# Kernel optimization log

Hardware: AMD Instinct MI355X
Metric: run time of the kernel (lower is better)

## Reference

```python
import jax, jax.numpy as jnp
import numpy as np

N_NODES = 100000
N_EDGES = 1200000
IN_DIM, HID_DIM, LAT_DIM = 128, 64, 32


def gcn_conv(x, W, b, src, dst, n_nodes):
    # PyG GCNConv with add_self_loops=True, symmetric normalization.
    # src/dst already include self loops.
    h = x @ W  # [N, out]
    deg = jax.ops.segment_sum(jnp.ones_like(dst, dtype=h.dtype), dst,
                              num_segments=n_nodes)  # includes self loop -> >=1
    dinv = jax.lax.rsqrt(deg)
    norm = dinv[src] * dinv[dst]  # [E]
    msg = h[src] * norm[:, None]  # gather + scale, [E, out]
    out = jax.ops.segment_sum(msg, dst, num_segments=n_nodes)  # scatter-add
    return out + b


def setup_inputs() -> dict:
    key = jax.random.key(0)
    ks = jax.random.split(key, 9)
    x = jax.random.normal(ks[0], (N_NODES, IN_DIM), dtype=jnp.float32)
    edge_index = jax.random.randint(ks[1], (2, N_EDGES), 0, N_NODES, dtype=jnp.int32)
    s1 = 1.0 / np.sqrt(IN_DIM)
    s2 = 1.0 / np.sqrt(HID_DIM)
    W1 = jax.random.uniform(ks[2], (IN_DIM, HID_DIM), jnp.float32, -s1, s1)
    b1 = jnp.zeros((HID_DIM,), jnp.float32)
    Wm = jax.random.uniform(ks[3], (HID_DIM, LAT_DIM), jnp.float32, -s2, s2)
    bm = jnp.zeros((LAT_DIM,), jnp.float32)
    Wv = jax.random.uniform(ks[4], (HID_DIM, LAT_DIM), jnp.float32, -s2, s2)
    bv = jnp.zeros((LAT_DIM,), jnp.float32)
    noise = jax.random.normal(ks[5], (N_NODES, LAT_DIM), dtype=jnp.float32)
    return {"x": x, "edge_index": edge_index, "W1": W1, "b1": b1,
            "Wm": Wm, "bm": bm, "Wv": Wv, "bv": bv, "noise": noise}


def reference(x, edge_index, W1, b1, Wm, bm, Wv, bv, noise):
    n = x.shape[0]
    loops = jnp.arange(n, dtype=edge_index.dtype)
    src = jnp.concatenate([edge_index[0], loops])
    dst = jnp.concatenate([edge_index[1], loops])
    h = jnp.tanh(gcn_conv(x, W1, b1, src, dst, n))
    mean = gcn_conv(h, Wm, bm, src, dst, n)
    logvar = gcn_conv(h, Wv, bv, src, dst, n)
    z = noise * jnp.exp(0.5 * logvar) + mean
    return (z, mean, logvar)
```

## Files before the change

kernel.cpp:

```cpp
#include <hip/hip_runtime.h>
#include <math.h>

#define TILE 4096
#define CSHIFT 11
#define CMASK 2047
#define NCMAX 64

typedef __attribute__((ext_vector_type(8))) short bf16x8;
typedef __attribute__((ext_vector_type(4))) float f32x4;


__device__ __forceinline__ unsigned int pack_bf16(float a, float b) {
  unsigned int ua = __float_as_uint(a);
  ua += 0x7FFFu + ((ua >> 16) & 1u);
  unsigned int ub = __float_as_uint(b);
  ub += 0x7FFFu + ((ub >> 16) & 1u);
  return (ua >> 16) | (ub & 0xFFFF0000u);
}

__device__ __forceinline__ void add8(float* acc, uint4 hv) {
  unsigned int u[4] = {hv.x, hv.y, hv.z, hv.w};
#pragma unroll
  for (int i = 0; i < 4; ++i) {
    acc[2 * i]     += __uint_as_float(u[i] << 16);
    acc[2 * i + 1] += __uint_as_float(u[i] & 0xFFFF0000u);
  }
}

__device__ __forceinline__ void fma4(float4& acc, float s, const float4& w) {
  acc.x = fmaf(s, w.x, acc.x);
  acc.y = fmaf(s, w.y, acc.y);
  acc.z = fmaf(s, w.z, acc.z);
  acc.w = fmaf(s, w.w, acc.w);
}


__global__ void zero_kernel(int* __restrict__ p, int n) {
  int i = blockIdx.x * blockDim.x + threadIdx.x;
  if (i < n) p[i] = 0;
}

__global__ __launch_bounds__(256) void coarse_hist_kernel(const int* __restrict__ dst,
    int* __restrict__ ccnt, int e) {
  __shared__ int h[NCMAX];
  if (threadIdx.x < NCMAX) h[threadIdx.x] = 0;
  __syncthreads();
  for (int i = blockIdx.x * 256 + threadIdx.x; i < e; i += gridDim.x * 256)
    atomicAdd(&h[dst[i] >> CSHIFT], 1);
  __syncthreads();
  if (threadIdx.x < NCMAX && h[threadIdx.x])
    atomicAdd(&ccnt[threadIdx.x * 16], h[threadIdx.x]);
}

__global__ __launch_bounds__(64) void coarse_scan_kernel(const int* __restrict__ ccnt,
    int* __restrict__ coff, int* __restrict__ ccur, int* __restrict__ off,
    int nc, int n, int e) {
  int t = threadIdx.x;
  int v = (t < nc) ? ccnt[t * 16] : 0;
  int incl = v;
#pragma unroll
  for (int ofs = 1; ofs < 64; ofs <<= 1) {
    int w = __shfl_up(incl, ofs);
    if (t >= ofs) incl += w;
  }
  int excl = incl - v;
  if (t < nc) { coff[t] = excl; ccur[t * 16] = excl; }
  if (t == nc - 1) coff[nc] = incl;
  if (t == 0) off[n] = e;
}

__global__ __launch_bounds__(256) void coarse_partition_kernel(const int* __restrict__ src,
    const int* __restrict__ dst, int* __restrict__ ccur,
    unsigned int* __restrict__ packed, int e) {
  __shared__ unsigned int stage[TILE];
  __shared__ unsigned char bid[TILE];
  __shared__ int hist[NCMAX], excl[NCMAX], gbase[NCMAX], lcur[NCMAX];
  int ntiles = (e + TILE - 1) / TILE;
  for (int tile = blockIdx.x; tile < ntiles; tile += gridDim.x) {
    int i0 = tile * TILE;
    int cnt = e - i0; if (cnt > TILE) cnt = TILE;
    if (threadIdx.x < NCMAX) hist[threadIdx.x] = 0;
    __syncthreads();
    int myS[16], myD[16];
#pragma unroll
    for (int k = 0; k < 16; ++k) {
      int li = threadIdx.x + k * 256;
      if (li < cnt) {
        myS[k] = src[i0 + li];
        myD[k] = dst[i0 + li];
        atomicAdd(&hist[myD[k] >> CSHIFT], 1);
      }
    }
    __syncthreads();
    if (threadIdx.x < NCMAX) {
      int t = threadIdx.x;
      int v = hist[t];
      int incl = v;
#pragma unroll
      for (int ofs = 1; ofs < 64; ofs <<= 1) {
        int w = __shfl_up(incl, ofs);
        if (t >= ofs) incl += w;
      }
      excl[t] = incl - v;
      lcur[t] = incl - v;
    }
    __syncthreads();
#pragma unroll
    for (int k = 0; k < 16; ++k) {
      int li = threadIdx.x + k * 256;
      if (li < cnt) {
        int c = myD[k] >> CSHIFT;
        int p = atomicAdd(&lcur[c], 1);
        stage[p] = (unsigned int)myS[k] | ((unsigned int)(myD[k] & CMASK) << 17);
        bid[p] = (unsigned char)c;
      }
    }
    __syncthreads();
    if (threadIdx.x < NCMAX) {
      int t = threadIdx.x;
      int cc = lcur[t] - excl[t];
      gbase[t] = cc ? atomicAdd(&ccur[t * 16], cc) : 0;
    }
    __syncthreads();
    for (int i = threadIdx.x; i < cnt; i += 256) {
      int c = bid[i];
      packed[gbase[c] + (i - excl[c])] = stage[i];
    }
    __syncthreads();
  }
}

__global__ __launch_bounds__(512) void csr_fine_kernel(const unsigned int* __restrict__ packed,
    const int* __restrict__ coff, int* __restrict__ off, float* __restrict__ dinv,
    int* __restrict__ csr, int n) {
  __shared__ int lh[2048];
  __shared__ int lsum[512];
  int b = blockIdx.x;
  int t = threadIdx.x;
  int e0 = coff[b], e1 = coff[b + 1];
  int node0 = b << CSHIFT;
  for (int i = t; i < 2048; i += 512) lh[i] = 0;
  __syncthreads();
  for (int i = e0 + t; i < e1; i += 512) atomicAdd(&lh[packed[i] >> 17], 1);
  __syncthreads();
  int base = t * 4;
  int v0 = lh[base], v1 = lh[base + 1], v2 = lh[base + 2], v3 = lh[base + 3];
  int tsum = v0 + v1 + v2 + v3;
  lsum[t] = tsum;
  __syncthreads();
  for (int ofs = 1; ofs < 512; ofs <<= 1) {
    int add = (t >= ofs) ? lsum[t - ofs] : 0;
    __syncthreads();
    lsum[t] += add;
    __syncthreads();
  }
  int ex = lsum[t] - tsum;
  int exc0 = ex, exc1 = ex + v0, exc2 = ex + v0 + v1, exc3 = ex + v0 + v1 + v2;
  lh[base] = exc0; lh[base + 1] = exc1; lh[base + 2] = exc2; lh[base + 3] = exc3;
  int node = node0 + base;
  if (node < n)     { off[node]     = e0 + exc0; dinv[node]     = rsqrtf((float)(v0 + 1)); }
  if (node + 1 < n) { off[node + 1] = e0 + exc1; dinv[node + 1] = rsqrtf((float)(v1 + 1)); }
  if (node + 2 < n) { off[node + 2] = e0 + exc2; dinv[node + 2] = rsqrtf((float)(v2 + 1)); }
  if (node + 3 < n) { off[node + 3] = e0 + exc3; dinv[node + 3] = rsqrtf((float)(v3 + 1)); }
  __syncthreads();
  for (int i = e0 + t; i < e1; i += 512) {
    unsigned int p = packed[i];
    int nl = p >> 17;
    int pos = atomicAdd(&lh[nl], 1);
    csr[e0 + pos] = (int)(p & 0x1FFFFu);
  }
}

__global__ __launch_bounds__(256) void gemm1_kernel(const float* __restrict__ x,
    const float* __restrict__ W1, const float* __restrict__ dinv,
    unsigned int* __restrict__ h1, int n) {
  __shared__ unsigned int xs[64 * 64];
  __shared__ unsigned int wt[64 * 64];
  for (int i = threadIdx.x; i < 4096; i += 256) {
    int c = i & 63, kp = i >> 6;
    float a = W1[(2 * kp) * 64 + c];
    float b = W1[(2 * kp + 1) * 64 + c];
    int slot = kp >> 2;
    int slotS = slot ^ (c & 7);
    wt[c * 64 + slotS * 4 + (kp & 3)] = pack_bf16(a, b);
  }
  int row0 = blockIdx.x * 64;
  int nrow = n - row0; if (nrow > 64) nrow = 64;
  for (int i = threadIdx.x; i < 64 * 32; i += 256) {
    int r = i >> 5, q = i & 31;
    float4 v = make_float4(0.f, 0.f, 0.f, 0.f);
    if (r < nrow) v = ((const float4*)(x + (size_t)(row0 + r) * 128))[q];
    int slot = q >> 1;
    int slotS = slot ^ (r & 7);
    int bi = r * 64 + slotS * 4 + (q & 1) * 2;
    xs[bi]     = pack_bf16(v.x, v.y);
    xs[bi + 1] = pack_bf16(v.z, v.w);
  }
  __syncthreads();
  int lane = threadIdx.x & 63;
  int w = threadIdx.x >> 6;
  int rl = lane & 15;
  int g = lane >> 4;
  f32x4 acc[4];
#pragma unroll
  for (int i = 0; i < 4; ++i) acc[i] = (f32x4){0.f, 0.f, 0.f, 0.f};
#pragma unroll
  for (int ks = 0; ks < 4; ++ks) {
    int as = ((ks * 4 + g) ^ (rl & 7)) * 4;
    bf16x8 af = *reinterpret_cast<const bf16x8*>(&xs[(w * 16 + rl) * 64 + as]);
#pragma unroll
    for (int nt = 0; nt < 4; ++nt) {
      int col = nt * 16 + rl;
      int bs = ((ks * 4 + g) ^ (col & 7)) * 4;
      bf16x8 bfr = *reinterpret_cast<const bf16x8*>(&wt[col * 64 + bs]);
      acc[nt] = __builtin_amdgcn_mfma_f32_16x16x32_bf16(af, bfr, acc[nt], 0, 0, 0);
    }
  }
#pragma unroll
  for (int i = 0; i < 4; ++i) {
    int row = row0 + w * 16 + g * 4 + i;
    float dv = (row < n) ? dinv[row] : 0.f;
#pragma unroll
    for (int nt = 0; nt < 4; ++nt) {
      float val = dv * acc[nt][i];
      float pv = __shfl_xor(val, 1);
      if (!(lane & 1) && row < n) {
        h1[(size_t)row * 32 + nt * 8 + (rl >> 1)] = pack_bf16(val, pv);
      }
    }
  }
}

template <int EPI>
__global__ __launch_bounds__(256) void agg_kernel(const uint4* __restrict__ h4,
    const int* __restrict__ off, const int* __restrict__ csr,
    const float* __restrict__ dinv, const float* __restrict__ bias,
    unsigned int* __restrict__ out, int n) {
  int lane = threadIdx.x & 63;
  int nd = lane >> 5;
  int j  = (lane >> 1) & 15;
  int fl = lane & 1;
  int node = blockIdx.x * 8 + (threadIdx.x >> 6) * 2 + nd;
  bool valid = node < n;
  float acc[32];
#pragma unroll
  for (int i = 0; i < 32; ++i) acc[i] = 0.f;
  if (valid) {
    if (j == 0) {
      const uint4* hp = &h4[(size_t)node * 8 + fl * 4];
      uint4 a = hp[0], b = hp[1], c = hp[2], d = hp[3];
      add8(acc, a); add8(acc + 8, b); add8(acc + 16, c); add8(acc + 24, d);
    }
    int e1 = off[node + 1];
    for (int ee = off[node] + j; ee < e1; ee += 16) {
      int s = __builtin_nontemporal_load(&csr[ee]);
      const uint4* hp = &h4[(size_t)s * 8 + fl * 4];
      uint4 a = hp[0], b = hp[1], c = hp[2], d = hp[3];
      add8(acc, a); add8(acc + 8, b); add8(acc + 16, c); add8(acc + 24, d);
    }
  }
#pragma unroll
  for (int i = 0; i < 16; ++i) {
    float tlo = acc[i]      + __shfl_xor(acc[i], 2);
    float thi = acc[i + 16] + __shfl_xor(acc[i + 16], 2);
    acc[i] = (j & 1) ? thi : tlo;
  }
#pragma unroll
  for (int i = 0; i < 8; ++i) {
    float tlo = acc[i]     + __shfl_xor(acc[i], 4);
    float thi = acc[i + 8] + __shfl_xor(acc[i + 8], 4);
    acc[i] = (j & 2) ? thi : tlo;
  }
#pragma unroll
  for (int i = 0; i < 4; ++i) {
    float tlo = acc[i]     + __shfl_xor(acc[i], 8);
    float thi = acc[i + 4] + __shfl_xor(acc[i + 4], 8);
    acc[i] = (j & 4) ? thi : tlo;
  }
#pragma unroll
  for (int i = 0; i < 2; ++i) {
    float tlo = acc[i]     + __shfl_xor(acc[i], 16);
    float thi = acc[i + 2] + __shfl_xor(acc[i + 2], 16);
    acc[i] = (j & 8) ? thi : tlo;
  }
  int b0 = j & 1, b1 = (j >> 1) & 1, b2 = (j >> 2) & 1, b3 = (j >> 3) & 1;
  int f0 = fl * 32 + 16 * b0 + 8 * b1 + 4 * b2 + 2 * b3;
  if (valid) {
    float di = dinv[node];
    float v0, v1;
    if (EPI) {
      v0 = di * tanhf(fmaf(di, acc[0], bias[f0]));
      v1 = di * tanhf(fmaf(di, acc[1], bias[f0 + 1]));
    } else {
      v0 = di * acc[0];
      v1 = di * acc[1];
    }
    out[(size_t)node * 32 + (f0 >> 1)] = pack_bf16(v0, v1);
  }
}

__global__ __launch_bounds__(256) void final_kernel(const unsigned int* __restrict__ aggb,
    const float* __restrict__ Wm, const float* __restrict__ bm,
    const float* __restrict__ Wv, const float* __restrict__ bv,
    const float* __restrict__ noise, float* __restrict__ outZ,
    float* __restrict__ outM, float* __restrict__ outLv, int n) {
  __shared__ float WmS[64 * 32];
  __shared__ float WvS[64 * 32];
  __shared__ float aggS[64 * 68];
  for (int i = threadIdx.x; i < 64 * 8; i += 256) {
    ((float4*)WmS)[i] = ((const float4*)Wm)[i];
    ((float4*)WvS)[i] = ((const float4*)Wv)[i];
  }
  int row0 = blockIdx.x * 64;
  int nrow = n - row0; if (nrow > 64) nrow = 64;
  for (int i = threadIdx.x; i < 64 * 16; i += 256) {
    int r = i >> 4, g = i & 15;
    uint2 u = make_uint2(0u, 0u);
    if (r < nrow) u = ((const uint2*)aggb)[(size_t)(row0 + r) * 16 + g];
    float* d = &aggS[r * 68 + g * 4];
    d[0] = __uint_as_float(u.x << 16);
    d[1] = __uint_as_float(u.x & 0xFFFF0000u);
    d[2] = __uint_as_float(u.y << 16);
    d[3] = __uint_as_float(u.y & 0xFFFF0000u);
  }
  __syncthreads();
  int c4 = (threadIdx.x & 7) * 4;
  int r2 = (threadIdx.x >> 3) * 2;
  float4 am[2], av[2];
#pragma unroll
  for (int i = 0; i < 2; ++i) {
    am[i] = make_float4(0.f, 0.f, 0.f, 0.f);
    av[i] = make_float4(0.f, 0.f, 0.f, 0.f);
  }
#pragma unroll 4
  for (int kq = 0; kq < 16; ++kq) {
    float4 xa[2], wm[4], wv[4];
#pragma unroll
    for (int i = 0; i < 2; ++i) xa[i] = *(const float4*)&aggS[(r2 + i) * 68 + kq * 4];
#pragma unroll
    for (int q = 0; q < 4; ++q) {
      wm[q] = *(const float4*)&WmS[(kq * 4 + q) * 32 + c4];
      wv[q] = *(const float4*)&WvS[(kq * 4 + q) * 32 + c4];
    }
#pragma unroll
    for (int i = 0; i < 2; ++i) {
      fma4(am[i], xa[i].x, wm[0]); fma4(am[i], xa[i].y, wm[1]);
      fma4(am[i], xa[i].z, wm[2]); fma4(am[i], xa[i].w, wm[3]);
      fma4(av[i], xa[i].x, wv[0]); fma4(av[i], xa[i].y, wv[1]);
      fma4(av[i], xa[i].z, wv[2]); fma4(av[i], xa[i].w, wv[3]);
    }
  }
  float4 bmv = *(const float4*)&bm[c4];
  float4 bvv = *(const float4*)&bv[c4];
#pragma unroll
  for (int i = 0; i < 2; ++i) {
    int row = row0 + r2 + i;
    if (row < n) {
      float4 m = am[i]; m.x += bmv.x; m.y += bmv.y; m.z += bmv.z; m.w += bmv.w;
      float4 v = av[i]; v.x += bvv.x; v.y += bvv.y; v.z += bvv.z; v.w += bvv.w;
      size_t oi = (size_t)row * 8 + (threadIdx.x & 7);
      float4 nz = ((const float4*)noise)[oi];
      float4 z;
      z.x = fmaf(nz.x, expf(0.5f * v.x), m.x);
      z.y = fmaf(nz.y, expf(0.5f * v.y), m.y);
      z.z = fmaf(nz.z, expf(0.5f * v.z), m.z);
      z.w = fmaf(nz.w, expf(0.5f * v.w), m.w);
      ((float4*)outZ)[oi] = z;
      ((float4*)outM)[oi] = m;
      ((float4*)outLv)[oi] = v;
    }
  }
}


extern "C" void kernel_launch(void* const* d_in, const int* in_sizes, int n_in,
                              void* d_out, int out_size, void* d_ws, size_t ws_size,
                              hipStream_t stream) {
  const float* x     = (const float*)d_in[0];
  const int*   edge  = (const int*)d_in[1];
  const float* W1    = (const float*)d_in[2];
  const float* b1    = (const float*)d_in[3];
  const float* Wm    = (const float*)d_in[4];
  const float* bm    = (const float*)d_in[5];
  const float* Wv    = (const float*)d_in[6];
  const float* bv    = (const float*)d_in[7];
  const float* noise = (const float*)d_in[8];
  int n = in_sizes[0] / 128;
  int e = in_sizes[1] / 2;
  const int* src = edge;
  const int* dst = edge + e;
  int nc = (n + CMASK) >> CSHIFT;

  int* ccnt = (int*)d_ws;
  int* ccur = ccnt + NCMAX * 16;
  int* coff = ccur + NCMAX * 16;
  int* off  = coff + (NCMAX + 4);
  float* dinv = (float*)(off + ((n + 4) & ~3));
  unsigned int* packed = (unsigned int*)(dinv + ((n + 3) & ~3));
  int* csr  = (int*)(packed + ((e + 3) & ~3));
  unsigned int* h1b = (unsigned int*)(csr + ((e + 3) & ~3));
  unsigned int* hb  = h1b + (size_t)n * 32;
  unsigned int* aggb = hb + (size_t)n * 32;

  float* outZ  = (float*)d_out;
  float* outM  = outZ + (size_t)n * 32;
  float* outLv = outM + (size_t)n * 32;

  int ntiles = (e + TILE - 1) / TILE;

  zero_kernel<<<(NCMAX * 16 + 255) / 256, 256, 0, stream>>>(ccnt, NCMAX * 16);
  coarse_hist_kernel<<<256, 256, 0, stream>>>(dst, ccnt, e);
  coarse_scan_kernel<<<1, 64, 0, stream>>>(ccnt, coff, ccur, off, nc, n, e);
  coarse_partition_kernel<<<ntiles, 256, 0, stream>>>(src, dst, ccur, packed, e);
  csr_fine_kernel<<<nc, 512, 0, stream>>>(packed, coff, off, dinv, csr, n);
  gemm1_kernel<<<(n + 63) / 64, 256, 0, stream>>>(x, W1, dinv, h1b, n);
  agg_kernel<1><<<(n + 7) / 8, 256, 0, stream>>>((const uint4*)h1b, off, csr, dinv, b1, hb, n);
  agg_kernel<0><<<(n + 7) / 8, 256, 0, stream>>>((const uint4*)hb, off, csr, dinv, b1, aggb, n);
  final_kernel<<<(n + 63) / 64, 256, 0, stream>>>(aggb, Wm, bm, Wv, bv, noise, outZ, outM, outLv, n);
}
```

Measured before the change: 192.8 us.

## Store hidden activations as FP8 for second aggregation and replicate histogram bins

```diff
diff --git a/kernel.cpp b/kernel.cpp
--- a/kernel.cpp
+++ b/kernel.cpp
@@ -8,6 +8,7 @@
 
 typedef __attribute__((ext_vector_type(8))) short bf16x8;
 typedef __attribute__((ext_vector_type(4))) float f32x4;
+typedef __attribute__((ext_vector_type(2))) float f32x2;
 
 
 __device__ __forceinline__ unsigned int pack_bf16(float a, float b) {
@@ -27,6 +28,19 @@
   }
 }
 
+__device__ __forceinline__ void add16_fp8(float* acc, uint4 hv) {
+  unsigned int u[4] = {hv.x, hv.y, hv.z, hv.w};
+#pragma unroll
+  for (int i = 0; i < 4; ++i) {
+    f32x2 lo = __builtin_amdgcn_cvt_pk_f32_fp8(u[i], false);
+    f32x2 hi = __builtin_amdgcn_cvt_pk_f32_fp8(u[i], true);
+    acc[4 * i + 0] += lo[0];
+    acc[4 * i + 1] += lo[1];
+    acc[4 * i + 2] += hi[0];
+    acc[4 * i + 3] += hi[1];
+  }
+}
+
 __device__ __forceinline__ void fma4(float4& acc, float s, const float4& w) {
   acc.x = fmaf(s, w.x, acc.x);
   acc.y = fmaf(s, w.y, acc.y);
@@ -42,14 +56,17 @@
 
 __global__ __launch_bounds__(256) void coarse_hist_kernel(const int* __restrict__ dst,
     int* __restrict__ ccnt, int e) {
-  __shared__ int h[NCMAX];
-  if (threadIdx.x < NCMAX) h[threadIdx.x] = 0;
-  __syncthreads();
+  __shared__ int h[NCMAX * 4];
+  for (int i = threadIdx.x; i < NCMAX * 4; i += 256) h[i] = 0;
+  __syncthreads();
+  int rep = threadIdx.x & 3;
   for (int i = blockIdx.x * 256 + threadIdx.x; i < e; i += gridDim.x * 256)
-    atomicAdd(&h[dst[i] >> CSHIFT], 1);
-  __syncthreads();
-  if (threadIdx.x < NCMAX && h[threadIdx.x])
-    atomicAdd(&ccnt[threadIdx.x * 16], h[threadIdx.x]);
+    atomicAdd(&h[((dst[i] >> CSHIFT) << 2) | rep], 1);
+  __syncthreads();
+  for (int i = threadIdx.x; i < NCMAX; i += 256) {
+    int s = h[i * 4] + h[i * 4 + 1] + h[i * 4 + 2] + h[i * 4 + 3];
+    if (s) atomicAdd(&ccnt[i * 16], s);
+  }
 }
 
 __global__ __launch_bounds__(64) void coarse_scan_kernel(const int* __restrict__ ccnt,
@@ -231,7 +248,7 @@
   }
 }
 
-template <int EPI>
+template <int EPI, int FP8IN>
 __global__ __launch_bounds__(256) void agg_kernel(const uint4* __restrict__ h4,
     const int* __restrict__ off, const int* __restrict__ csr,
     const float* __restrict__ dinv, const float* __restrict__ bias,
@@ -247,16 +264,28 @@
   for (int i = 0; i < 32; ++i) acc[i] = 0.f;
   if (valid) {
     if (j == 0) {
-      const uint4* hp = &h4[(size_t)node * 8 + fl * 4];
-      uint4 a = hp[0], b = hp[1], c = hp[2], d = hp[3];
-      add8(acc, a); add8(acc + 8, b); add8(acc + 16, c); add8(acc + 24, d);
+      if (FP8IN) {
+        const uint4* hp = &h4[(size_t)node * 4 + fl * 2];
+        uint4 a = hp[0], b = hp[1];
+        add16_fp8(acc, a); add16_fp8(acc + 16, b);
+      } else {
+        const uint4* hp = &h4[(size_t)node * 8 + fl * 4];
+        uint4 a = hp[0], b = hp[1], c = hp[2], d = hp[3];
+        add8(acc, a); add8(acc + 8, b); add8(acc + 16, c); add8(acc + 24, d);
+      }
     }
     int e1 = off[node + 1];
     for (int ee = off[node] + j; ee < e1; ee += 16) {
       int s = __builtin_nontemporal_load(&csr[ee]);
-      const uint4* hp = &h4[(size_t)s * 8 + fl * 4];
-      uint4 a = hp[0], b = hp[1], c = hp[2], d = hp[3];
-      add8(acc, a); add8(acc + 8, b); add8(acc + 16, c); add8(acc + 24, d);
+      if (FP8IN) {
+        const uint4* hp = &h4[(size_t)s * 4 + fl * 2];
+        uint4 a = hp[0], b = hp[1];
+        add16_fp8(acc, a); add16_fp8(acc + 16, b);
+      } else {
+        const uint4* hp = &h4[(size_t)s * 8 + fl * 4];
+        uint4 a = hp[0], b = hp[1], c = hp[2], d = hp[3];
+        add8(acc, a); add8(acc + 8, b); add8(acc + 16, c); add8(acc + 24, d);
+      }
     }
   }
 #pragma unroll
@@ -287,15 +316,16 @@
   int f0 = fl * 32 + 16 * b0 + 8 * b1 + 4 * b2 + 2 * b3;
   if (valid) {
     float di = dinv[node];
-    float v0, v1;
     if (EPI) {
-      v0 = di * tanhf(fmaf(di, acc[0], bias[f0]));
-      v1 = di * tanhf(fmaf(di, acc[1], bias[f0 + 1]));
+      float v0 = di * tanhf(fmaf(di, acc[0], bias[f0]));
+      float v1 = di * tanhf(fmaf(di, acc[1], bias[f0 + 1]));
+      unsigned int pk = __builtin_amdgcn_cvt_pk_fp8_f32(v0, v1, 0u, false);
+      ((unsigned short*)out)[(size_t)node * 32 + (f0 >> 1)] = (unsigned short)pk;
     } else {
-      v0 = di * acc[0];
-      v1 = di * acc[1];
-    }
-    out[(size_t)node * 32 + (f0 >> 1)] = pack_bf16(v0, v1);
+      float v0 = di * acc[0];
+      float v1 = di * acc[1];
+      out[(size_t)node * 32 + (f0 >> 1)] = pack_bf16(v0, v1);
+    }
   }
 }
 
@@ -400,7 +430,7 @@
   int* csr  = (int*)(packed + ((e + 3) & ~3));
   unsigned int* h1b = (unsigned int*)(csr + ((e + 3) & ~3));
   unsigned int* hb  = h1b + (size_t)n * 32;
-  unsigned int* aggb = hb + (size_t)n * 32;
+  unsigned int* aggb = hb + (size_t)n * 16;
 
   float* outZ  = (float*)d_out;
   float* outM  = outZ + (size_t)n * 32;
@@ -409,12 +439,12 @@
   int ntiles = (e + TILE - 1) / TILE;
 
   zero_kernel<<<(NCMAX * 16 + 255) / 256, 256, 0, stream>>>(ccnt, NCMAX * 16);
-  coarse_hist_kernel<<<256, 256, 0, stream>>>(dst, ccnt, e);
+  coarse_hist_kernel<<<512, 256, 0, stream>>>(dst, ccnt, e);
   coarse_scan_kernel<<<1, 64, 0, stream>>>(ccnt, coff, ccur, off, nc, n, e);
   coarse_partition_kernel<<<ntiles, 256, 0, stream>>>(src, dst, ccur, packed, e);
   csr_fine_kernel<<<nc, 512, 0, stream>>>(packed, coff, off, dinv, csr, n);
   gemm1_kernel<<<(n + 63) / 64, 256, 0, stream>>>(x, W1, dinv, h1b, n);
-  agg_kernel<1><<<(n + 7) / 8, 256, 0, stream>>>((const uint4*)h1b, off, csr, dinv, b1, hb, n);
-  agg_kernel<0><<<(n + 7) / 8, 256, 0, stream>>>((const uint4*)hb, off, csr, dinv, b1, aggb, n);
+  agg_kernel<1, 0><<<(n + 7) / 8, 256, 0, stream>>>((const uint4*)h1b, off, csr, dinv, b1, hb, n);
+  agg_kernel<0, 1><<<(n + 7) / 8, 256, 0, stream>>>((const uint4*)hb, off, csr, dinv, b1, aggb, n);
   final_kernel<<<(n + 63) / 64, 256, 0, stream>>>(aggb, Wm, bm, Wv, bv, noise, outZ, outM, outLv, n);
 }
```

Result: no change. 190.6 us (-1.1%).
